# Performance work log

Hardware: AMD Instinct MI355X
Metric: run time of the kernel (lower is better)

The kernel has to match this reference:

```python
import jax, jax.numpy as jnp
import numpy as np
from jax import lax

TOP_K = 8

B, S, D, N, R = 32, 128, 512, 131072, 16


def setup_inputs() -> dict:
    key = jax.random.key(0)
    ks = jax.random.split(key, 10)
    return {
        "query": jax.random.normal(ks[0], (B, S, D), jnp.float32),
        "base_memory": jax.random.normal(ks[1], (N, D), jnp.float32) * 0.01,
        "lora_A": jax.random.normal(ks[2], (N, R), jnp.float32) * 0.01,
        "lora_B": jax.random.normal(ks[3], (R, D), jnp.float32) * 0.01,
        "gru_w_ih": jax.random.normal(ks[4], (3 * D, D), jnp.float32) * 0.02,
        "gru_w_hh": jax.random.normal(ks[5], (3 * D, D), jnp.float32) * 0.02,
        "gru_b_ih": jax.random.normal(ks[6], (3 * D,), jnp.float32) * 0.02,
        "gru_b_hh": jax.random.normal(ks[7], (3 * D,), jnpp.float32) if False else jax.random.normal(ks[7], (3 * D,), jnp.float32) * 0.02,
        "wg_w": jax.random.normal(ks[8], (1, D), jnp.float32) * 0.02,
        "wg_b": jnp.zeros((1,), jnp.float32),
    }


def gru_cell(x, h, w_ih, w_hh, b_ih, b_hh):
    # torch.nn.GRUCell math; gates ordered [r, z, n]
    gx = x @ w_ih.T + b_ih            # [B, 3D]
    gh = h @ w_hh.T + b_hh            # [B, 3D]
    gx_r, gx_z, gx_n = jnp.split(gx, 3, axis=-1)
    gh_r, gh_z, gh_n = jnp.split(gh, 3, axis=-1)
    r = jax.nn.sigmoid(gx_r + gh_r)
    z = jax.nn.sigmoid(gx_z + gh_z)
    n = jnp.tanh(gx_n + r * gh_n)
    return (1.0 - z) * n + z * h


def reference(query, base_memory, lora_A, lora_B, gru_w_ih, gru_w_hh, gru_b_ih, gru_b_hh, wg_w, wg_b):
    mem = base_memory + lora_A @ lora_B                 # [N, D]
    q = query.mean(axis=1)                              # [B, D]
    scores = q @ mem.T                                  # [B, N]
    top_scores, top_idx = lax.top_k(scores, TOP_K)      # [B, K]
    retrieved = mem[top_idx]                            # [B, K, D] gather

    h0 = jnp.zeros_like(q)
    hidden = gru_cell(retrieved.sum(axis=1), h0, gru_w_ih, gru_w_hh, gru_b_ih, gru_b_hh)

    write_prob = jax.nn.sigmoid(hidden @ wg_w.T + wg_b)  # [B, 1]
    value = q                                            # value[b, 0] in torch == q[b]

    # Sequential over batch (matches torch loop order); within a batch the
    # top-k indices are distinct so a vectorized scatter-set is exact.
    def step(m, inp):
        idx, p, v = inp                                  # [K], scalar, [D]
        rows = (1.0 - p) * m[idx] + p * v
        return m.at[idx].set(rows), None

    new_mem, _ = lax.scan(step, base_memory, (top_idx, write_prob[:, 0], value))
    return retrieved, hidden, new_mem
```

## Files before the change

kernel.cpp:

```cpp
#include <hip/hip_runtime.h>
#include <math.h>

#define NROWS 131072
#define DDIM  512
#define BB    32
#define SS    128
#define KK    8

__global__ __launch_bounds__(256) void k_qmean(const float* __restrict__ query,
                                               float* __restrict__ q) {
  int idx = blockIdx.x * 256 + threadIdx.x;
  int b = idx >> 9, d = idx & 511;
  const float* p = query + (size_t)b * SS * DDIM + d;
  float s = 0.f;
  #pragma unroll 8
  for (int i = 0; i < SS; ++i) s += p[(size_t)i * DDIM];
  q[idx] = s * (1.0f / 128.0f);
}

__global__ __launch_bounds__(256) void k_mem(const float* __restrict__ base,
                                             const float* __restrict__ A,
                                             const float* __restrict__ Bm,
                                             float* __restrict__ newmem) {
  int gt = blockIdx.x * 256 + threadIdx.x;
  int c = gt & 127;
  int stream = gt >> 7;
  int row0 = stream * 64;
  int srow0 = __builtin_amdgcn_readfirstlane(row0);

  float4 Breg[16];
  #pragma unroll
  for (int r = 0; r < 16; ++r)
    Breg[r] = *(const float4*)(Bm + r * DDIM + 4 * c);

  #pragma unroll 4
  for (int i = 0; i < 64; ++i) {
    int n = row0 + i;
    const float* Ar = A + (size_t)(srow0 + i) * 16;
    float4 acc = *(const float4*)(base + (size_t)n * DDIM + 4 * c);
    #pragma unroll
    for (int r = 0; r < 16; ++r) {
      float a = Ar[r];
      acc.x += a * Breg[r].x; acc.y += a * Breg[r].y;
      acc.z += a * Breg[r].z; acc.w += a * Breg[r].w;
    }
    *(float4*)(newmem + (size_t)n * DDIM + 4 * c) = acc;
  }
}

__global__ __launch_bounds__(256) void k_scores(const float* __restrict__ mem,
                                                const float* __restrict__ q,
                                                float* __restrict__ scores) {
  __shared__ float4 sq[4096];
  int t = threadIdx.x;
  const float4* qg = (const float4*)q;
  #pragma unroll
  for (int u = 0; u < 16; ++u) sq[u * 256 + t] = qg[u * 256 + t];
  __syncthreads();

  int r = blockIdx.x * 256 + t;
  float acc[32];
  #pragma unroll
  for (int b = 0; b < 32; ++b) acc[b] = 0.f;
  const float4* mrow = (const float4*)(mem + (size_t)r * DDIM);
  #pragma unroll 2
  for (int d4 = 0; d4 < 128; ++d4) {
    float4 v = mrow[d4];
    #pragma unroll
    for (int b = 0; b < 32; ++b) {
      float4 qv = sq[b * 128 + d4];
      acc[b] += qv.x*v.x + qv.y*v.y + qv.z*v.z + qv.w*v.w;
    }
  }
  #pragma unroll
  for (int b = 0; b < 32; ++b) scores[(size_t)b * NROWS + r] = acc[b];
}

__device__ __forceinline__ void insert8(float (&v)[8], int (&ix)[8], float x, int i) {
  bool better = (x > v[7]) || (x == v[7] && i < ix[7]);
  if (!better) return;
  v[7] = x; ix[7] = i;
  #pragma unroll
  for (int u = 7; u > 0; --u) {
    bool sw = (v[u] > v[u-1]) || (v[u] == v[u-1] && ix[u] < ix[u-1]);
    if (sw) {
      float tv = v[u]; v[u] = v[u-1]; v[u-1] = tv;
      int ti = ix[u]; ix[u] = ix[u-1]; ix[u-1] = ti;
    }
  }
}

__global__ __launch_bounds__(256) void k_topk1(const float* __restrict__ scores,
                                               float* __restrict__ cval,
                                               int* __restrict__ cidx) {
  __shared__ float lval[256][8]; __shared__ int lidx[256][8];
  __shared__ float mval[32][8];  __shared__ int midx[32][8];
  int b = blockIdx.x >> 4, j = blockIdx.x & 15, t = threadIdx.x;
  const float4* s4 = (const float4*)(scores + (size_t)b * NROWS + j * 8192);

  float v[8]; int ix[8];
  #pragma unroll
  for (int e = 0; e < 8; ++e) { v[e] = -1e30f; ix[e] = 0x7fffffff; }
  #pragma unroll
  for (int i = 0; i < 8; ++i) {
    int f4 = i * 256 + t;
    float4 x = s4[f4];
    int n0 = j * 8192 + f4 * 4;
    insert8(v, ix, x.x, n0);
    insert8(v, ix, x.y, n0 + 1);
    insert8(v, ix, x.z, n0 + 2);
    insert8(v, ix, x.w, n0 + 3);
  }
  #pragma unroll
  for (int e = 0; e < 8; ++e) { lval[t][e] = v[e]; lidx[t][e] = ix[e]; }
  __syncthreads();

  if (t < 32) {
    float mv[8]; int mi[8];
    #pragma unroll
    for (int e = 0; e < 8; ++e) { mv[e] = -1e30f; mi[e] = 0x7fffffff; }
    for (int u = 0; u < 8; ++u) {
      int src = t * 8 + u;
      #pragma unroll
      for (int e = 0; e < 8; ++e) insert8(mv, mi, lval[src][e], lidx[src][e]);
    }
    #pragma unroll
    for (int e = 0; e < 8; ++e) { mval[t][e] = mv[e]; midx[t][e] = mi[e]; }
  }
  __syncthreads();

  if (t == 0) {
    float mv[8]; int mi[8];
    #pragma unroll
    for (int e = 0; e < 8; ++e) { mv[e] = -1e30f; mi[e] = 0x7fffffff; }
    for (int u = 0; u < 32; ++u)
      #pragma unroll
      for (int e = 0; e < 8; ++e) insert8(mv, mi, mval[u][e], midx[u][e]);
    #pragma unroll
    for (int e = 0; e < 8; ++e) {
      cval[(b * 16 + j) * 8 + e] = mv[e];
      cidx[(b * 16 + j) * 8 + e] = mi[e];
    }
  }
}

__global__ __launch_bounds__(128) void k_gather(const float* __restrict__ mem,
                                                const float* __restrict__ cval,
                                                const int* __restrict__ cidx,
                                                int* __restrict__ topidx,
                                                float* __restrict__ retrieved,
                                                float* __restrict__ x) {
  __shared__ float scv[128]; __shared__ int sci[128];
  __shared__ int stop[8];
  int b = blockIdx.x, t = threadIdx.x;
  scv[t] = cval[b * 128 + t];
  sci[t] = cidx[b * 128 + t];
  __syncthreads();
  if (t == 0) {
    float mv[8]; int mi[8];
    #pragma unroll
    for (int e = 0; e < 8; ++e) { mv[e] = -1e30f; mi[e] = 0x7fffffff; }
    for (int u = 0; u < 128; ++u) insert8(mv, mi, scv[u], sci[u]);
    #pragma unroll
    for (int e = 0; e < 8; ++e) { stop[e] = mi[e]; topidx[b * 8 + e] = mi[e]; }
  }
  __syncthreads();

  float4 xs = make_float4(0.f, 0.f, 0.f, 0.f);
  #pragma unroll
  for (int k = 0; k < 8; ++k) {
    int row = stop[k];
    float4 vv = *(const float4*)(mem + (size_t)row * DDIM + 4 * t);
    *(float4*)(retrieved + (size_t)(b * 8 + k) * DDIM + 4 * t) = vv;
    xs.x += vv.x; xs.y += vv.y; xs.z += vv.z; xs.w += vv.w;
  }
  *(float4*)(x + (size_t)b * DDIM + 4 * t) = xs;
}

__global__ __launch_bounds__(512) void k_gru(const float* __restrict__ x,
                                             const float* __restrict__ wih,
                                             const float* __restrict__ bih,
                                             const float* __restrict__ bhh,
                                             const float* __restrict__ wgw,
                                             const float* __restrict__ wgb,
                                             float* __restrict__ hidden,
                                             float* __restrict__ pws) {
  __shared__ float sx[512];
  __shared__ float sred[8];
  int b = blockIdx.x, t = threadIdx.x;
  sx[t] = x[b * 512 + t];
  __syncthreads();
  const float* wr = wih + (size_t)t * 512;
  const float* wz = wih + (size_t)(512 + t) * 512;
  const float* wn = wih + (size_t)(1024 + t) * 512;
  float gr = 0.f, gz = 0.f, gn = 0.f;
  #pragma unroll 4
  for (int d4 = 0; d4 < 128; ++d4) {
    float4 xv = *(const float4*)(sx + 4 * d4);
    float4 a = *(const float4*)(wr + 4 * d4);
    float4 c = *(const float4*)(wz + 4 * d4);
    float4 e = *(const float4*)(wn + 4 * d4);
    gr += a.x*xv.x + a.y*xv.y + a.z*xv.z + a.w*xv.w;
    gz += c.x*xv.x + c.y*xv.y + c.z*xv.z + c.w*xv.w;
    gn += e.x*xv.x + e.y*xv.y + e.z*xv.z + e.w*xv.w;
  }
  float r = 1.f / (1.f + expf(-(gr + bih[t]        + bhh[t])));
  float z = 1.f / (1.f + expf(-(gz + bih[512 + t]  + bhh[512 + t])));
  float n = tanhf(gn + bih[1024 + t] + r * bhh[1024 + t]);
  float h = (1.f - z) * n;
  hidden[b * 512 + t] = h;

  float pw = h * wgw[t];
  #pragma unroll
  for (int off = 32; off > 0; off >>= 1) pw += __shfl_down(pw, off, 64);
  if ((t & 63) == 0) sred[t >> 6] = pw;
  __syncthreads();
  if (t == 0) {
    float ssum = 0.f;
    #pragma unroll
    for (int j = 0; j < 8; ++j) ssum += sred[j];
    pws[b] = 1.f / (1.f + expf(-(ssum + wgb[0])));
  }
}

__global__ __launch_bounds__(256) void k_scatter(float* __restrict__ newmem,
                                                 const int* __restrict__ topidx,
                                                 const float* __restrict__ pws,
                                                 const float* __restrict__ q) {
  int t = threadIdx.x;
  int d = blockIdx.x * 64 + (t & 63);
  int k0 = t >> 6;
  for (int b = 0; b < 32; ++b) {
    float p = pws[b];
    float qv = q[b * 512 + d];
    #pragma unroll
    for (int kk = 0; kk < 2; ++kk) {
      int k = k0 + kk * 4;
      int row = topidx[b * 8 + k];
      size_t off = (size_t)row * 512 + d;
      float m = __hip_atomic_load(newmem + off, __ATOMIC_RELAXED,
                                  __HIP_MEMORY_SCOPE_AGENT);
      __hip_atomic_store(newmem + off, (1.f - p) * m + p * qv,
                         __ATOMIC_RELAXED, __HIP_MEMORY_SCOPE_AGENT);
    }
    __syncthreads();
  }
}

extern "C" void kernel_launch(void* const* d_in, const int* in_sizes, int n_in,
                              void* d_out, int out_size, void* d_ws, size_t ws_size,
                              hipStream_t stream) {
  const float* query = (const float*)d_in[0];
  const float* base  = (const float*)d_in[1];
  const float* lA    = (const float*)d_in[2];
  const float* lB    = (const float*)d_in[3];
  const float* wih   = (const float*)d_in[4];
  const float* bih   = (const float*)d_in[6];
  const float* bhh   = (const float*)d_in[7];
  const float* wgw   = (const float*)d_in[8];
  const float* wgb   = (const float*)d_in[9];

  float* out = (float*)d_out;
  float* retrieved = out;
  float* hidden    = out + 131072;
  float* newmem    = out + 147456;

  float* wq  = (float*)d_ws;
  float* wsc = wq + 16384;
  float* wx  = wsc + 4194304;
  float* wp  = wx + 16384;
  int*   wti = (int*)(wp + 32);
  float* wcv = (float*)(wti + 256);
  int*   wci = (int*)(wcv + 4096);

  k_qmean  <<<64,   256, 0, stream>>>(query, wq);
  k_mem    <<<1024, 256, 0, stream>>>(base, lA, lB, newmem);
  k_scores <<<512,  256, 0, stream>>>(newmem, wq, wsc);
  k_topk1  <<<512,  256, 0, stream>>>(wsc, wcv, wci);
  k_gather <<<32,   128, 0, stream>>>(newmem, wcv, wci, wti, retrieved, wx);
  k_gru    <<<32,   512, 0, stream>>>(wx, wih, bih, bhh, wgw, wgb, hidden, wp);
  k_scatter<<<8,    256, 0, stream>>>(newmem, wti, wp, wq);
}
```

Baseline: 951.5 us.

## Parallelize qmean and GRU across more blocks, prefetch rows in mem and scores

k_qmean now splits each batch's sequence reduction across 256 blocks and combines partial sums in shared memory. k_gru is spread over 256 small blocks that accumulate the write-gate dot product with atomics, and the sigmoid moves into k_scatter. k_mem and k_scores gain software prefetching of the next rows, and k_scores gives each thread two rows so every shared q load feeds more FMAs. Doubling the accumulators in k_scores raises register pressure and may reduce occupancy, and atomicAdd makes the write-gate sum order nondeterministic.

```diff
diff --git a/kernel.cpp b/kernel.cpp
--- a/kernel.cpp
+++ b/kernel.cpp
@@ -8,14 +8,26 @@
 #define KK    8
 
 __global__ __launch_bounds__(256) void k_qmean(const float* __restrict__ query,
-                                               float* __restrict__ q) {
-  int idx = blockIdx.x * 256 + threadIdx.x;
-  int b = idx >> 9, d = idx & 511;
-  const float* p = query + (size_t)b * SS * DDIM + d;
+                                               float* __restrict__ q,
+                                               float* __restrict__ pwsum) {
+  __shared__ float part[256];
+  int b  = blockIdx.x >> 3;
+  int dc = blockIdx.x & 7;
+  int t  = threadIdx.x;
+  if (blockIdx.x == 0 && t < 32) pwsum[t] = 0.f;
+  int lane = t & 63;
+  int p    = t >> 6;
+  const float* src = query + (size_t)b * SS * DDIM + (size_t)(p * 32) * DDIM
+                   + dc * 64 + lane;
   float s = 0.f;
   #pragma unroll 8
-  for (int i = 0; i < SS; ++i) s += p[(size_t)i * DDIM];
-  q[idx] = s * (1.0f / 128.0f);
+  for (int i = 0; i < 32; ++i) s += src[(size_t)i * DDIM];
+  part[t] = s;
+  __syncthreads();
+  if (t < 64) {
+    float tot = part[t] + part[64 + t] + part[128 + t] + part[192 + t];
+    q[b * DDIM + dc * 64 + t] = tot * (1.0f / 128.0f);
+  }
 }
 
 __global__ __launch_bounds__(256) void k_mem(const float* __restrict__ base,
@@ -33,18 +45,35 @@
   for (int r = 0; r < 16; ++r)
     Breg[r] = *(const float4*)(Bm + r * DDIM + 4 * c);
 
-  #pragma unroll 4
-  for (int i = 0; i < 64; ++i) {
-    int n = row0 + i;
-    const float* Ar = A + (size_t)(srow0 + i) * 16;
-    float4 acc = *(const float4*)(base + (size_t)n * DDIM + 4 * c);
-    #pragma unroll
-    for (int r = 0; r < 16; ++r) {
-      float a = Ar[r];
-      acc.x += a * Breg[r].x; acc.y += a * Breg[r].y;
-      acc.z += a * Breg[r].z; acc.w += a * Breg[r].w;
-    }
-    *(float4*)(newmem + (size_t)n * DDIM + 4 * c) = acc;
+  const float* bp = base   + (size_t)row0 * DDIM + 4 * c;
+  float*       np = newmem + (size_t)row0 * DDIM + 4 * c;
+
+  float4 nxt0 = *(const float4*)(bp);
+  float4 nxt1 = *(const float4*)(bp + DDIM);
+  float4 nxt2 = *(const float4*)(bp + 2 * DDIM);
+  float4 nxt3 = *(const float4*)(bp + 3 * DDIM);
+
+  for (int i = 0; i < 64; i += 4) {
+    float4 cur0 = nxt0, cur1 = nxt1, cur2 = nxt2, cur3 = nxt3;
+    if (i + 4 < 64) {
+      const float* p = bp + (size_t)(i + 4) * DDIM;
+      nxt0 = *(const float4*)(p);
+      nxt1 = *(const float4*)(p + DDIM);
+      nxt2 = *(const float4*)(p + 2 * DDIM);
+      nxt3 = *(const float4*)(p + 3 * DDIM);
+    }
+    #pragma unroll
+    for (int k = 0; k < 4; ++k) {
+      const float* Ar = A + (size_t)(srow0 + i + k) * 16;
+      float4 acc = (k == 0) ? cur0 : (k == 1) ? cur1 : (k == 2) ? cur2 : cur3;
+      #pragma unroll
+      for (int r = 0; r < 16; ++r) {
+        float a = Ar[r];
+        acc.x += a * Breg[r].x; acc.y += a * Breg[r].y;
+        acc.z += a * Breg[r].z; acc.w += a * Breg[r].w;
+      }
+      *(float4*)(np + (size_t)(i + k) * DDIM) = acc;
+    }
   }
 }
 
@@ -58,22 +87,45 @@
   for (int u = 0; u < 16; ++u) sq[u * 256 + t] = qg[u * 256 + t];
   __syncthreads();
 
-  int r = blockIdx.x * 256 + t;
-  float acc[32];
-  #pragma unroll
-  for (int b = 0; b < 32; ++b) acc[b] = 0.f;
-  const float4* mrow = (const float4*)(mem + (size_t)r * DDIM);
-  #pragma unroll 2
-  for (int d4 = 0; d4 < 128; ++d4) {
-    float4 v = mrow[d4];
-    #pragma unroll
-    for (int b = 0; b < 32; ++b) {
-      float4 qv = sq[b * 128 + d4];
-      acc[b] += qv.x*v.x + qv.y*v.y + qv.z*v.z + qv.w*v.w;
-    }
-  }
-  #pragma unroll
-  for (int b = 0; b < 32; ++b) scores[(size_t)b * NROWS + r] = acc[b];
+  int r0 = blockIdx.x * 512 + t;
+  float acc0[32], acc1[32];
+  #pragma unroll
+  for (int b = 0; b < 32; ++b) { acc0[b] = 0.f; acc1[b] = 0.f; }
+
+  const float4* m0 = (const float4*)(mem + (size_t)r0 * DDIM);
+  const float4* m1 = (const float4*)(mem + (size_t)(r0 + 256) * DDIM);
+
+  float4 a_nxt0 = m0[0], a_nxt1 = m0[1], a_nxt2 = m0[2], a_nxt3 = m0[3];
+  float4 b_nxt0 = m1[0], b_nxt1 = m1[1], b_nxt2 = m1[2], b_nxt3 = m1[3];
+
+  for (int g = 0; g < 32; ++g) {
+    float4 a0 = a_nxt0, a1 = a_nxt1, a2 = a_nxt2, a3 = a_nxt3;
+    float4 c0 = b_nxt0, c1 = b_nxt1, c2 = b_nxt2, c3 = b_nxt3;
+    if (g < 31) {
+      int nb = 4 * (g + 1);
+      a_nxt0 = m0[nb];     a_nxt1 = m0[nb + 1];
+      a_nxt2 = m0[nb + 2]; a_nxt3 = m0[nb + 3];
+      b_nxt0 = m1[nb];     b_nxt1 = m1[nb + 1];
+      b_nxt2 = m1[nb + 2]; b_nxt3 = m1[nb + 3];
+    }
+    #pragma unroll
+    for (int j = 0; j < 4; ++j) {
+      int d4 = 4 * g + j;
+      float4 x0 = (j == 0) ? a0 : (j == 1) ? a1 : (j == 2) ? a2 : a3;
+      float4 x1 = (j == 0) ? c0 : (j == 1) ? c1 : (j == 2) ? c2 : c3;
+      #pragma unroll
+      for (int b = 0; b < 32; ++b) {
+        float4 qv = sq[b * 128 + d4];
+        acc0[b] += qv.x*x0.x + qv.y*x0.y + qv.z*x0.z + qv.w*x0.w;
+        acc1[b] += qv.x*x1.x + qv.y*x1.y + qv.z*x1.z + qv.w*x1.w;
+      }
+    }
+  }
+  #pragma unroll
+  for (int b = 0; b < 32; ++b) {
+    scores[(size_t)b * NROWS + r0]       = acc0[b];
+    scores[(size_t)b * NROWS + r0 + 256] = acc1[b];
+  }
 }
 
 __device__ __forceinline__ void insert8(float (&v)[8], int (&ix)[8], float x, int i) {
@@ -177,26 +229,24 @@
   *(float4*)(x + (size_t)b * DDIM + 4 * t) = xs;
 }
 
-__global__ __launch_bounds__(512) void k_gru(const float* __restrict__ x,
-                                             const float* __restrict__ wih,
-                                             const float* __restrict__ bih,
-                                             const float* __restrict__ bhh,
-                                             const float* __restrict__ wgw,
-                                             const float* __restrict__ wgb,
-                                             float* __restrict__ hidden,
-                                             float* __restrict__ pws) {
-  __shared__ float sx[512];
-  __shared__ float sred[8];
-  int b = blockIdx.x, t = threadIdx.x;
-  sx[t] = x[b * 512 + t];
-  __syncthreads();
+__global__ __launch_bounds__(64) void k_gru(const float* __restrict__ x,
+                                            const float* __restrict__ wih,
+                                            const float* __restrict__ bih,
+                                            const float* __restrict__ bhh,
+                                            const float* __restrict__ wgw,
+                                            float* __restrict__ hidden,
+                                            float* __restrict__ pwsum) {
+  int b     = blockIdx.x >> 3;
+  int chunk = blockIdx.x & 7;
+  int t = chunk * 64 + threadIdx.x;
+  const float* xb = x + b * 512;
   const float* wr = wih + (size_t)t * 512;
   const float* wz = wih + (size_t)(512 + t) * 512;
   const float* wn = wih + (size_t)(1024 + t) * 512;
   float gr = 0.f, gz = 0.f, gn = 0.f;
   #pragma unroll 4
   for (int d4 = 0; d4 < 128; ++d4) {
-    float4 xv = *(const float4*)(sx + 4 * d4);
+    float4 xv = *(const float4*)(xb + 4 * d4);
     float4 a = *(const float4*)(wr + 4 * d4);
     float4 c = *(const float4*)(wz + 4 * d4);
     float4 e = *(const float4*)(wn + 4 * d4);
@@ -213,25 +263,19 @@
   float pw = h * wgw[t];
   #pragma unroll
   for (int off = 32; off > 0; off >>= 1) pw += __shfl_down(pw, off, 64);
-  if ((t & 63) == 0) sred[t >> 6] = pw;
-  __syncthreads();
-  if (t == 0) {
-    float ssum = 0.f;
-    #pragma unroll
-    for (int j = 0; j < 8; ++j) ssum += sred[j];
-    pws[b] = 1.f / (1.f + expf(-(ssum + wgb[0])));
-  }
+  if (threadIdx.x == 0) atomicAdd(pwsum + b, pw);
 }
 
 __global__ __launch_bounds__(256) void k_scatter(float* __restrict__ newmem,
                                                  const int* __restrict__ topidx,
-                                                 const float* __restrict__ pws,
+                                                 const float* __restrict__ pwsum,
+                                                 const float* __restrict__ wgb,
                                                  const float* __restrict__ q) {
   int t = threadIdx.x;
   int d = blockIdx.x * 64 + (t & 63);
   int k0 = t >> 6;
   for (int b = 0; b < 32; ++b) {
-    float p = pws[b];
+    float p = 1.f / (1.f + expf(-(pwsum[b] + wgb[0])));
     float qv = q[b * 512 + d];
     #pragma unroll
     for (int kk = 0; kk < 2; ++kk) {
@@ -273,11 +317,11 @@
   float* wcv = (float*)(wti + 256);
   int*   wci = (int*)(wcv + 4096);
 
-  k_qmean  <<<64,   256, 0, stream>>>(query, wq);
+  k_qmean  <<<256,  256, 0, stream>>>(query, wq, wp);
   k_mem    <<<1024, 256, 0, stream>>>(base, lA, lB, newmem);
-  k_scores <<<512,  256, 0, stream>>>(newmem, wq, wsc);
+  k_scores <<<256,  256, 0, stream>>>(newmem, wq, wsc);
   k_topk1  <<<512,  256, 0, stream>>>(wsc, wcv, wci);
   k_gather <<<32,   128, 0, stream>>>(newmem, wcv, wci, wti, retrieved, wx);
-  k_gru    <<<32,   512, 0, stream>>>(wx, wih, bih, bhh, wgw, wgb, hidden, wp);
-  k_scatter<<<8,    256, 0, stream>>>(newmem, wti, wp, wq);
-}
+  k_gru    <<<256,  64,  0, stream>>>(wx, wih, bih, bhh, wgw, hidden, wp);
+  k_scatter<<<8,    256, 0, stream>>>(newmem, wti, wp, wgb, wq);
+}
```

Result: faster. 881.7 us (-7.3%).
